# Optimization experiments

Measured on AMD Instinct MI355X. Metric: run time of the kernel, lower is better.

## Reference

```python
import jax, jax.numpy as jnp
import numpy as np

N, IN_FT, OUT_FT = 10000, 512, 256


def setup_inputs() -> dict:
    key = jax.random.key(0)
    k1, k2, k3 = jax.random.split(key, 3)
    feat = jax.random.normal(k1, (N, IN_FT), dtype=jnp.float32)
    adj = jax.random.uniform(k2, (N, N), dtype=jnp.float32)  # nonneg edge weights
    W = jax.random.normal(k3, (IN_FT, OUT_FT), dtype=jnp.float32) * 0.05
    conv_bias = jnp.zeros((OUT_FT,), dtype=jnp.float32)
    extra_bias = jnp.zeros((OUT_FT,), dtype=jnp.float32)
    return {"feat": feat, "adj": adj, "W": W,
            "conv_bias": conv_bias, "extra_bias": extra_bias}


def reference(feat, adj, W, conv_bias, extra_bias):
    n = adj.shape[0]
    idx = jnp.arange(n)
    # gcn_norm: fill_diag(adj, 1.0) -> self loops with weight 1 on the diagonal
    A_hat = adj.at[idx, idx].set(1.0)  # [N, N]
    deg = A_hat.sum(axis=1)            # row degree
    dinv = jnp.where(deg > 0, jax.lax.rsqrt(deg), 0.0)  # D^-1/2
    # linear transform first (standard GCNConv order), then normalized aggregation
    h = feat @ W                                   # [N, OUT_FT]
    # D^-1/2 A_hat D^-1/2 h, fused as row/col scalings to avoid a second NxN buffer
    agg = dinv[:, None] * (A_hat @ (dinv[:, None] * h))
    out = agg + conv_bias + extra_bias
    return jax.nn.relu(out)
```

## Files before the change

kernel.cpp:

```cpp
#include <hip/hip_runtime.h>

#define NROW 10000
#define NF 256
#define KF 512
#define MP 10048
#define NTILES 157

typedef __attribute__((ext_vector_type(8))) short short8x;
typedef __attribute__((ext_vector_type(4))) float f32x4;

__device__ __forceinline__ unsigned int bf16rne(float f){
  unsigned int u = __builtin_bit_cast(unsigned int, f);
  u += 0x7fffu + ((u >> 16) & 1u);
  return u >> 16;
}

__global__ void k_zero(float4* __restrict__ p){
  p[blockIdx.x * 256 + threadIdx.x] = make_float4(0.f, 0.f, 0.f, 0.f);
}

__global__ __launch_bounds__(256) void k_prep3(const float* __restrict__ adj,
        unsigned short* __restrict__ adjb, float* __restrict__ degp){
  int t = threadIdx.x, lane = t & 63;
  int row = blockIdx.x * 4 + (t >> 6);
  const f32x4* src = (const f32x4*)(adj + (size_t)row * NROW);
  unsigned short* dst = adjb + (size_t)row * MP;
  const f32x4 zero4 = {0.f, 0.f, 0.f, 0.f};
  f32x4 sacc = zero4;

  for (int it = 0; it < 5; ++it){
    int base = it * 512 + lane * 2;
    f32x4 v[8];
    #pragma unroll
    for (int s = 0; s < 4; ++s){
      int fi = base + s * 128;
      v[2*s]   = (fi     < 2500) ? __builtin_nontemporal_load(src + fi)     : zero4;
      v[2*s+1] = (fi + 1 < 2500) ? __builtin_nontemporal_load(src + fi + 1) : zero4;
    }
    #pragma unroll
    for (int s = 0; s < 4; ++s){
      int fi = base + s * 128;
      int gc0 = fi * 4, gc1 = gc0 + 4;
      f32x4 w0 = v[2*s], w1 = v[2*s+1];
      if (row == gc0    ) w0[0] = 1.f;
      if (row == gc0 + 1) w0[1] = 1.f;
      if (row == gc0 + 2) w0[2] = 1.f;
      if (row == gc0 + 3) w0[3] = 1.f;
      if (row == gc1    ) w1[0] = 1.f;
      if (row == gc1 + 1) w1[1] = 1.f;
      if (row == gc1 + 2) w1[2] = 1.f;
      if (row == gc1 + 3) w1[3] = 1.f;
      sacc += w0; sacc += w1;
      uint4 o;
      o.x = bf16rne(w0[0]) | (bf16rne(w0[1]) << 16);
      o.y = bf16rne(w0[2]) | (bf16rne(w0[3]) << 16);
      o.z = bf16rne(w1[0]) | (bf16rne(w1[1]) << 16);
      o.w = bf16rne(w1[2]) | (bf16rne(w1[3]) << 16);
      if (fi < 2512) *(uint4*)(dst + gc0) = o;
    }
  }
  float s = (sacc[0] + sacc[1]) + (sacc[2] + sacc[3]);
  #pragma unroll
  for (int off = 32; off; off >>= 1) s += __shfl_down(s, off);
  if (lane == 0) degp[row] = s;
}

__global__ void k_dinv(const float* __restrict__ degp, float* __restrict__ dinv,
                       unsigned short* __restrict__ hsT){
  int i = blockIdx.x * 256 + threadIdx.x;
  if (i >= MP) return;
  float d = 0.f;
  if (i < NROW){
    float tot = degp[i];
    d = tot > 0.f ? rsqrtf(tot) : 0.f;
  }
  dinv[i] = d;
  if (i < NF){
    unsigned int* tz = (unsigned int*)(hsT + (size_t)i * MP + NROW);
    #pragma unroll
    for (int m = 0; m < (MP - NROW) / 2; ++m) tz[m] = 0u;
  }
}

__global__ __launch_bounds__(128) void k_featw(const float* __restrict__ feat,
        const float* __restrict__ W, const float* __restrict__ dinv,
        unsigned short* __restrict__ hsT){
  __shared__ __align__(16) float fs[8][512];
  int t = threadIdx.x;
  int i0 = blockIdx.x * 8;
  #pragma unroll
  for (int it = 0; it < 8; ++it){
    int idx = it * 128 + t;
    int r = idx >> 7, c4 = (idx & 127) * 4;
    *(float4*)&fs[r][c4] = *(const float4*)(feat + (size_t)(i0 + r) * KF + c4);
  }
  __syncthreads();
  float acc[8][2];
  #pragma unroll
  for (int r = 0; r < 8; ++r){ acc[r][0] = 0.f; acc[r][1] = 0.f; }
  int c0 = t, c1 = t + 128;
  for (int k = 0; k < KF; k += 4){
    const float* Wk = W + (size_t)k * NF;
    float w0a = Wk[c0],        w0b = Wk[c1];
    float w1a = Wk[NF + c0],   w1b = Wk[NF + c1];
    float w2a = Wk[2*NF + c0], w2b = Wk[2*NF + c1];
    float w3a = Wk[3*NF + c0], w3b = Wk[3*NF + c1];
    #pragma unroll
    for (int r = 0; r < 8; ++r){
      float4 f = *(const float4*)&fs[r][k];
      float a0 = acc[r][0], a1 = acc[r][1];
      a0 = fmaf(f.x, w0a, a0); a1 = fmaf(f.x, w0b, a1);
      a0 = fmaf(f.y, w1a, a0); a1 = fmaf(f.y, w1b, a1);
      a0 = fmaf(f.z, w2a, a0); a1 = fmaf(f.z, w2b, a1);
      a0 = fmaf(f.w, w3a, a0); a1 = fmaf(f.w, w3b, a1);
      acc[r][0] = a0; acc[r][1] = a1;
    }
  }
  float dv[8];
  #pragma unroll
  for (int r = 0; r < 8; ++r) dv[r] = dinv[i0 + r];
  unsigned short* d0 = hsT + (size_t)c0 * MP + i0;
  unsigned short* d1 = hsT + (size_t)c1 * MP + i0;
  #pragma unroll
  for (int r = 0; r < 8; r += 2){
    unsigned int u0 = bf16rne(acc[r][0] * dv[r]) | (bf16rne(acc[r+1][0] * dv[r+1]) << 16);
    unsigned int u1 = bf16rne(acc[r][1] * dv[r]) | (bf16rne(acc[r+1][1] * dv[r+1]) << 16);
    *(unsigned int*)(d0 + r) = u0;
    *(unsigned int*)(d1 + r) = u1;
  }
}

__global__ __launch_bounds__(256, 3) void k_gemm(const unsigned short* __restrict__ adjb,
        const unsigned short* __restrict__ hsT, float* __restrict__ out){
  __shared__ __align__(16) unsigned short Al[64][72];
  __shared__ __align__(16) unsigned short Bl[256][72];
  int t = threadIdx.x;
  int lane = t & 63, wid = t >> 6;
  int wr = wid >> 1, wc = wid & 1;
  int r0 = blockIdx.x * 64;
  int by = blockIdx.y;
  int kt0 = by * 39 + (by > 0 ? 1 : 0);
  int kt1 = (by + 1) * 39 + 1;

  f32x4 acc[2][8];
  #pragma unroll
  for (int a = 0; a < 2; ++a)
    #pragma unroll
    for (int b = 0; b < 8; ++b)
      #pragma unroll
      for (int j = 0; j < 4; ++j) acc[a][b][j] = 0.f;

  int bcol = t >> 3;
  int bko  = (t & 7) * 8;

  for (int kt = kt0; kt < kt1; ++kt){
    int k0 = kt * 64;
    #pragma unroll
    for (int it = 0; it < 2; ++it){
      int slot = it * 256 + t;
      int row = slot >> 3, off8 = (slot & 7) * 8;
      *(uint4*)&Al[row][off8] =
          *(const uint4*)(adjb + (size_t)(r0 + row) * MP + k0 + off8);
    }
    #pragma unroll
    for (int it = 0; it < 8; ++it){
      int cc = it * 32 + bcol;
      *(uint4*)&Bl[cc][bko] = *(const uint4*)(hsT + (size_t)cc * MP + k0 + bko);
    }
    __syncthreads();
    #pragma unroll
    for (int kk = 0; kk < 64; kk += 32){
      short8x a0 = *(const short8x*)&Al[wr*32      + (lane & 15)][kk + (lane >> 4) * 8];
      short8x a1 = *(const short8x*)&Al[wr*32 + 16 + (lane & 15)][kk + (lane >> 4) * 8];
      #pragma unroll
      for (int ni = 0; ni < 8; ++ni){
        short8x b = *(const short8x*)&Bl[wc*128 + ni*16 + (lane & 15)][kk + (lane >> 4) * 8];
        acc[0][ni] = __builtin_amdgcn_mfma_f32_16x16x32_bf16(a0, b, acc[0][ni], 0, 0, 0);
        acc[1][ni] = __builtin_amdgcn_mfma_f32_16x16x32_bf16(a1, b, acc[1][ni], 0, 0, 0);
      }
    }
    __syncthreads();
  }
  #pragma unroll
  for (int mi = 0; mi < 2; ++mi){
    #pragma unroll
    for (int ni = 0; ni < 8; ++ni){
      int gc = wc*128 + ni*16 + (lane & 15);
      #pragma unroll
      for (int j = 0; j < 4; ++j){
        int gr = r0 + wr*32 + mi*16 + (lane >> 4) * 4 + j;
        if (gr < NROW) atomicAdd(out + (size_t)gr * NF + gc, acc[mi][ni][j]);
      }
    }
  }
}

__global__ void k_epi(float* __restrict__ out, const float* __restrict__ dinv,
                      const float* __restrict__ cb, const float* __restrict__ eb){
  int e = (blockIdx.x * 256 + threadIdx.x) * 4;
  int i = e >> 8, c = e & 255;
  float di = dinv[i];
  float4 v = *(float4*)(out + e);
  v.x = fmaxf(fmaf(v.x, di, cb[c+0] + eb[c+0]), 0.f);
  v.y = fmaxf(fmaf(v.y, di, cb[c+1] + eb[c+1]), 0.f);
  v.z = fmaxf(fmaf(v.z, di, cb[c+2] + eb[c+2]), 0.f);
  v.w = fmaxf(fmaf(v.w, di, cb[c+3] + eb[c+3]), 0.f);
  *(float4*)(out + e) = v;
}

extern "C" void kernel_launch(void* const* d_in, const int* in_sizes, int n_in,
                              void* d_out, int out_size, void* d_ws, size_t ws_size,
                              hipStream_t stream){
  const float* feat = (const float*)d_in[0];
  const float* adj  = (const float*)d_in[1];
  const float* W    = (const float*)d_in[2];
  const float* cb   = (const float*)d_in[3];
  const float* eb   = (const float*)d_in[4];
  float* out = (float*)d_out;

  float* degp = (float*)d_ws;
  float* dinv = (float*)((char*)d_ws + (256u << 10));
  unsigned short* hsT  = (unsigned short*)((char*)d_ws + (512u << 10));
  unsigned short* adjb = (unsigned short*)((char*)d_ws + (8u << 20));

  k_zero <<<(NROW*NF)/1024,  256, 0, stream>>>((float4*)out);
  k_prep3<<<NROW/4,          256, 0, stream>>>(adj, adjb, degp);
  k_dinv <<<(MP + 255)/256,  256, 0, stream>>>(degp, dinv, hsT);
  k_featw<<<NROW/8,          128, 0, stream>>>(feat, W, dinv, hsT);
  k_gemm <<<dim3(NTILES, 4), 256, 0, stream>>>(adjb, hsT, out);
  k_epi  <<<(NROW*NF)/1024,  256, 0, stream>>>(out, dinv, cb, eb);
}
```

Measured before the change: 281.4 us.

## Drop split-K atomics, use 32-row tiles with full K and fused epilogue

The GEMM now gives each block a 32-row tile over the full K range instead of 64-row tiles split four ways along K with atomicAdd. This removes the zeroing kernel, the atomics and the separate epilogue kernel, since dinv scaling, bias and ReLU are applied directly before the store. Manual bf16 rounding is also replaced with the HIP intrinsic. In exchange, each block reloads the whole B matrix per 32-row tile, which doubles B traffic, and the grid drops to 313 blocks, each running a longer K loop.

```diff
diff --git a/kernel.cpp b/kernel.cpp
--- a/kernel.cpp
+++ b/kernel.cpp
@@ -1,22 +1,21 @@
 #include <hip/hip_runtime.h>
+#include <hip/hip_bf16.h>
 
 #define NROW 10000
 #define NF 256
 #define KF 512
 #define MP 10048
-#define NTILES 157
+#define NKT 157
+#define NT32 313
 
 typedef __attribute__((ext_vector_type(8))) short short8x;
 typedef __attribute__((ext_vector_type(4))) float f32x4;
 
-__device__ __forceinline__ unsigned int bf16rne(float f){
-  unsigned int u = __builtin_bit_cast(unsigned int, f);
-  u += 0x7fffu + ((u >> 16) & 1u);
-  return u >> 16;
-}
-
-__global__ void k_zero(float4* __restrict__ p){
-  p[blockIdx.x * 256 + threadIdx.x] = make_float4(0.f, 0.f, 0.f, 0.f);
+__device__ __forceinline__ unsigned int pkbf16(float a, float b){
+  union { __hip_bfloat16 h[2]; unsigned int u; } cv;
+  cv.h[0] = __float2bfloat16(a);
+  cv.h[1] = __float2bfloat16(b);
+  return cv.u;
 }
 
 __global__ __launch_bounds__(256) void k_prep3(const float* __restrict__ adj,
@@ -52,10 +51,10 @@
       if (row == gc1 + 3) w1[3] = 1.f;
       sacc += w0; sacc += w1;
       uint4 o;
-      o.x = bf16rne(w0[0]) | (bf16rne(w0[1]) << 16);
-      o.y = bf16rne(w0[2]) | (bf16rne(w0[3]) << 16);
-      o.z = bf16rne(w1[0]) | (bf16rne(w1[1]) << 16);
-      o.w = bf16rne(w1[2]) | (bf16rne(w1[3]) << 16);
+      o.x = pkbf16(w0[0], w0[1]);
+      o.y = pkbf16(w0[2], w0[3]);
+      o.z = pkbf16(w1[0], w1[1]);
+      o.w = pkbf16(w1[2], w1[3]);
       if (fi < 2512) *(uint4*)(dst + gc0) = o;
     }
   }
@@ -123,45 +122,42 @@
   unsigned short* d1 = hsT + (size_t)c1 * MP + i0;
   #pragma unroll
   for (int r = 0; r < 8; r += 2){
-    unsigned int u0 = bf16rne(acc[r][0] * dv[r]) | (bf16rne(acc[r+1][0] * dv[r+1]) << 16);
-    unsigned int u1 = bf16rne(acc[r][1] * dv[r]) | (bf16rne(acc[r+1][1] * dv[r+1]) << 16);
+    unsigned int u0 = pkbf16(acc[r][0] * dv[r], acc[r+1][0] * dv[r+1]);
+    unsigned int u1 = pkbf16(acc[r][1] * dv[r], acc[r+1][1] * dv[r+1]);
     *(unsigned int*)(d0 + r) = u0;
     *(unsigned int*)(d1 + r) = u1;
   }
 }
 
 __global__ __launch_bounds__(256, 3) void k_gemm(const unsigned short* __restrict__ adjb,
-        const unsigned short* __restrict__ hsT, float* __restrict__ out){
-  __shared__ __align__(16) unsigned short Al[64][72];
+        const unsigned short* __restrict__ hsT, const float* __restrict__ dinv,
+        const float* __restrict__ cb, const float* __restrict__ eb,
+        float* __restrict__ out){
+  __shared__ __align__(16) unsigned short Al[32][72];
   __shared__ __align__(16) unsigned short Bl[256][72];
   int t = threadIdx.x;
   int lane = t & 63, wid = t >> 6;
-  int wr = wid >> 1, wc = wid & 1;
-  int r0 = blockIdx.x * 64;
-  int by = blockIdx.y;
-  int kt0 = by * 39 + (by > 0 ? 1 : 0);
-  int kt1 = (by + 1) * 39 + 1;
-
-  f32x4 acc[2][8];
+  int l15 = lane & 15, hi = lane >> 4;
+  int r0 = blockIdx.x * 32;
+
+  f32x4 acc[2][4];
   #pragma unroll
   for (int a = 0; a < 2; ++a)
     #pragma unroll
-    for (int b = 0; b < 8; ++b)
+    for (int b = 0; b < 4; ++b)
       #pragma unroll
       for (int j = 0; j < 4; ++j) acc[a][b][j] = 0.f;
 
+  int arow = t >> 3;
+  int aoff = (t & 7) * 8;
   int bcol = t >> 3;
   int bko  = (t & 7) * 8;
-
-  for (int kt = kt0; kt < kt1; ++kt){
+  int agr = r0 + arow; if (agr > NROW - 1) agr = NROW - 1;
+  const unsigned short* asrc = adjb + (size_t)agr * MP;
+
+  for (int kt = 0; kt < NKT; ++kt){
     int k0 = kt * 64;
-    #pragma unroll
-    for (int it = 0; it < 2; ++it){
-      int slot = it * 256 + t;
-      int row = slot >> 3, off8 = (slot & 7) * 8;
-      *(uint4*)&Al[row][off8] =
-          *(const uint4*)(adjb + (size_t)(r0 + row) * MP + k0 + off8);
-    }
+    *(uint4*)&Al[arow][aoff] = *(const uint4*)(asrc + k0 + aoff);
     #pragma unroll
     for (int it = 0; it < 8; ++it){
       int cc = it * 32 + bcol;
@@ -170,42 +166,40 @@
     __syncthreads();
     #pragma unroll
     for (int kk = 0; kk < 64; kk += 32){
-      short8x a0 = *(const short8x*)&Al[wr*32      + (lane & 15)][kk + (lane >> 4) * 8];
-      short8x a1 = *(const short8x*)&Al[wr*32 + 16 + (lane & 15)][kk + (lane >> 4) * 8];
+      short8x a0 = *(const short8x*)&Al[l15     ][kk + hi * 8];
+      short8x a1 = *(const short8x*)&Al[l15 + 16][kk + hi * 8];
       #pragma unroll
-      for (int ni = 0; ni < 8; ++ni){
-        short8x b = *(const short8x*)&Bl[wc*128 + ni*16 + (lane & 15)][kk + (lane >> 4) * 8];
+      for (int ni = 0; ni < 4; ++ni){
+        short8x b = *(const short8x*)&Bl[wid*64 + ni*16 + l15][kk + hi * 8];
         acc[0][ni] = __builtin_amdgcn_mfma_f32_16x16x32_bf16(a0, b, acc[0][ni], 0, 0, 0);
         acc[1][ni] = __builtin_amdgcn_mfma_f32_16x16x32_bf16(a1, b, acc[1][ni], 0, 0, 0);
       }
     }
     __syncthreads();
   }
-  #pragma unroll
-  for (int mi = 0; mi < 2; ++mi){
-    #pragma unroll
-    for (int ni = 0; ni < 8; ++ni){
-      int gc = wc*128 + ni*16 + (lane & 15);
+  float dv[2][4];
+  #pragma unroll
+  for (int mi = 0; mi < 2; ++mi)
+    #pragma unroll
+    for (int j = 0; j < 4; ++j){
+      int gr = r0 + mi*16 + hi*4 + j;
+      dv[mi][j] = (gr < NROW) ? dinv[gr] : 0.f;
+    }
+  #pragma unroll
+  for (int ni = 0; ni < 4; ++ni){
+    int gc = wid*64 + ni*16 + l15;
+    float bias = cb[gc] + eb[gc];
+    #pragma unroll
+    for (int mi = 0; mi < 2; ++mi){
       #pragma unroll
       for (int j = 0; j < 4; ++j){
-        int gr = r0 + wr*32 + mi*16 + (lane >> 4) * 4 + j;
-        if (gr < NROW) atomicAdd(out + (size_t)gr * NF + gc, acc[mi][ni][j]);
+        int gr = r0 + mi*16 + hi*4 + j;
+        if (gr < NROW)
+          out[(size_t)gr * NF + gc] =
+              fmaxf(fmaf(dv[mi][j], acc[mi][ni][j], bias), 0.f);
       }
     }
   }
-}
-
-__global__ void k_epi(float* __restrict__ out, const float* __restrict__ dinv,
-                      const float* __restrict__ cb, const float* __restrict__ eb){
-  int e = (blockIdx.x * 256 + threadIdx.x) * 4;
-  int i = e >> 8, c = e & 255;
-  float di = dinv[i];
-  float4 v = *(float4*)(out + e);
-  v.x = fmaxf(fmaf(v.x, di, cb[c+0] + eb[c+0]), 0.f);
-  v.y = fmaxf(fmaf(v.y, di, cb[c+1] + eb[c+1]), 0.f);
-  v.z = fmaxf(fmaf(v.z, di, cb[c+2] + eb[c+2]), 0.f);
-  v.w = fmaxf(fmaf(v.w, di, cb[c+3] + eb[c+3]), 0.f);
-  *(float4*)(out + e) = v;
 }
 
 extern "C" void kernel_launch(void* const* d_in, const int* in_sizes, int n_in,
@@ -223,10 +217,8 @@
   unsigned short* hsT  = (unsigned short*)((char*)d_ws + (512u << 10));
   unsigned short* adjb = (unsigned short*)((char*)d_ws + (8u << 20));
 
-  k_zero <<<(NROW*NF)/1024,  256, 0, stream>>>((float4*)out);
   k_prep3<<<NROW/4,          256, 0, stream>>>(adj, adjb, degp);
   k_dinv <<<(MP + 255)/256,  256, 0, stream>>>(degp, dinv, hsT);
   k_featw<<<NROW/8,          128, 0, stream>>>(feat, W, dinv, hsT);
-  k_gemm <<<dim3(NTILES, 4), 256, 0, stream>>>(adjb, hsT, out);
-  k_epi  <<<(NROW*NF)/1024,  256, 0, stream>>>(out, dinv, cb, eb);
-}
+  k_gemm <<<NT32,            256, 0, stream>>>(adjb, hsT, dinv, cb, eb, out);
+}
```

After: 338.4 us. +20.3%, slower.
